# Optimization experiments

Measured on AMD Instinct MI355X. Metric: run time of the kernel, lower is better.

Reference implementation:

```python
import jax, jax.numpy as jnp
import numpy as np

EMBED_DIM = 128
N_HEADS = 8
HEAD_DEPTH = EMBED_DIM // N_HEADS  # 16
CLIP = 10.0
B, N = 256, 1000


def setup_inputs() -> dict:
    key = jax.random.key(0)
    ks = jax.random.split(key, 10)
    D = EMBED_DIM
    return {
        "node_embeddings": jax.random.normal(ks[0], (B, N, D), jnp.float32),
        "graph_embedding": jax.random.normal(ks[1], (B, D), jnp.float32),
        "step_context": jax.random.normal(ks[2], (B, 1, D + 2), jnp.float32),
        "mask": jax.random.randint(ks[3], (B, 1, N), 0, 2).astype(bool),
        "Wk1": jax.random.normal(ks[4], (D, D), jnp.float32) / np.sqrt(D),
        "Wv": jax.random.normal(ks[5], (D, D), jnp.float32) / np.sqrt(D),
        "Wk2": jax.random.normal(ks[6], (D, D), jnp.float32) / np.sqrt(D),
        "Wq_fixed": jax.random.normal(ks[7], (D, D), jnp.float32) / np.sqrt(D),
        "Wout": jax.random.normal(ks[8], (D, D), jnp.float32) / np.sqrt(D),
        "Wq_step": jax.random.normal(ks[9], (D + 2, D), jnp.float32) / np.sqrt(D),
    }


def reference(node_embeddings, graph_embedding, step_context, mask,
              Wk1, Wv, Wk2, Wq_fixed, Wout, Wq_step):
    b, n, D = node_embeddings.shape
    H, dh = N_HEADS, HEAD_DEPTH
    neg_inf = jnp.float32(-1e9)

    # compute_static: precomputed projections of node/graph embeddings
    K1 = node_embeddings @ Wk1                      # [B,N,D]
    V = node_embeddings @ Wv                        # [B,N,D]
    K2 = node_embeddings @ Wk2                      # [B,N,D]
    Q_fixed = graph_embedding[:, None, :] @ Wq_fixed  # [B,1,D]

    # compute_dynamic: single-query masked MHA
    Q_step = step_context @ Wq_step                 # [B,1,D]
    Q1 = Q_fixed + Q_step                           # [B,1,D]
    q = Q1.reshape(b, 1, H, dh)
    k = K1.reshape(b, n, H, dh)
    v = V.reshape(b, n, H, dh)
    score = jnp.einsum('bqhd,bkhd->bhqk', q, k) / jnp.sqrt(jnp.float32(dh))
    score = jnp.where(mask[:, None, :, :], neg_inf, score)  # mask [B,1,N] -> [B,1,1,N]
    attn = jax.nn.softmax(score, axis=-1)           # [B,H,1,N]
    mha = jnp.einsum('bhqk,bkhd->bqhd', attn, v).reshape(b, 1, D)
    Q2 = mha @ Wout                                 # [B,1,D]

    # SHA: clipped single-head logits over all nodes
    logits = CLIP * jnp.tanh(
        jnp.einsum('bqd,bkd->bqk', Q2, K2) / jnp.sqrt(jnp.float32(D)))  # [B,1,N]
    logits = jnp.where(mask, neg_inf, logits)
    return logits[:, 0, :]                          # [B,N]
```

## Files before the change

### kernel.cpp

```cpp
#include <hip/hip_runtime.h>
#include <stdint.h>


#define DD 128
#define NH 8
#define DHD 16
#define NS 8
#define NMAX_PAD 1024
#define TILE 64
#define RP 132

__device__ __forceinline__ bool detect_mask32(const void* maskp) {
    const uint32_t* mw = (const uint32_t*)maskp;
    bool m32 = true;
    #pragma unroll
    for (int i = 0; i < 16; ++i) m32 = m32 && (mw[i] <= 1u);
    return m32;
}

__global__ __launch_bounds__(128)
void k0_prep(const float* __restrict__ graph, const float* __restrict__ ctx,
             const float* __restrict__ Wk1, const float* __restrict__ Wqf,
             const float* __restrict__ Wqs, float* __restrict__ wq_ws)
{
    __shared__ float q1[DD];
    const int b = blockIdx.x, tid = threadIdx.x;
    const float* ge = graph + (size_t)b * DD;
    const float* sc = ctx + (size_t)b * (DD + 2);
    float acc = 0.f;
    for (int k = 0; k < DD; ++k)     acc += ge[k] * Wqf[k * DD + tid];
    for (int k = 0; k < DD + 2; ++k) acc += sc[k] * Wqs[k * DD + tid];
    q1[tid] = acc;
    __syncthreads();
    const float* wrow = Wk1 + (size_t)tid * DD;
    #pragma unroll
    for (int h = 0; h < NH; ++h) {
        float a = 0.f;
        #pragma unroll
        for (int j = 0; j < DHD; ++j) a += wrow[h * DHD + j] * q1[h * DHD + j];
        wq_ws[(size_t)b * NH * DD + h * DD + tid] = 0.25f * a;
    }
}

__global__ __launch_bounds__(512)
void k1_scores(const float* __restrict__ node, const float* __restrict__ wq_ws,
               float* __restrict__ attn_ws, int N)
{
    __shared__ float tile[TILE * RP];
    __shared__ float wq_l[NH * RP];
    const int b = blockIdx.y, tid = threadIdx.x;
    const int base = blockIdx.x * 128;
    const float* nodeB = node + (size_t)b * N * DD;

    for (int i = tid; i < NH * DD; i += 512) {
        const int h = i >> 7, dp = i & 127;
        wq_l[h * RP + dp] = wq_ws[(size_t)b * NH * DD + h * DD + dp];
    }
    __syncthreads();

    const int n_local = tid >> 3, hA = tid & 7;
    for (int t = 0; t < 2; ++t) {
        const int n0 = base + t * TILE;
        #pragma unroll
        for (int c = 0; c < 4; ++c) {
            const int idx = c * (512 * 4) + tid * 4;
            const int row = idx >> 7, col = idx & 127;
            if (n0 + row < N)
                *(float4*)&tile[row * RP + col] =
                    *(const float4*)(nodeB + (size_t)(n0 + row) * DD + col);
        }
        __syncthreads();
        if (n0 + n_local < N) {
            const float4* nr = (const float4*)&tile[n_local * RP];
            const float4* wr = (const float4*)&wq_l[hA * RP];
            float acc = 0.f;
            #pragma unroll
            for (int k = 0; k < 32; ++k) {
                const float4 a = nr[k], w = wr[k];
                acc += a.x * w.x + a.y * w.y + a.z * w.z + a.w * w.w;
            }
            attn_ws[(size_t)b * NH * NMAX_PAD + hA * NMAX_PAD + (n0 + n_local)] = acc;
        }
        __syncthreads();
    }
}

__global__ __launch_bounds__(512)
void k2_softmax(const void* __restrict__ maskp, float* __restrict__ attn_ws, int N)
{
    const int b = blockIdx.x, tid = threadIdx.x, lane = tid & 63, h = tid >> 6;
    const bool m32 = detect_mask32(maskp);
    const int32_t* mi = (const int32_t*)maskp + (size_t)b * N;
    const uint8_t* mb = (const uint8_t*)maskp + (size_t)b * N;
    float* arow = attn_ws + (size_t)b * NH * NMAX_PAD + h * NMAX_PAD;

    float sm[16];
    #pragma unroll
    for (int k = 0; k < 16; ++k) {
        const int n = lane + 64 * k;
        float v = -1e30f;
        if (n < N) {
            const bool m = m32 ? (mi[n] != 0) : (mb[n] != 0);
            v = m ? -1e9f : arow[n];
        }
        sm[k] = v;
    }
    float mx = sm[0];
    #pragma unroll
    for (int k = 1; k < 16; ++k) mx = fmaxf(mx, sm[k]);
    #pragma unroll
    for (int d = 1; d < 64; d <<= 1) mx = fmaxf(mx, __shfl_xor(mx, d));
    float e[16], sum = 0.f;
    #pragma unroll
    for (int k = 0; k < 16; ++k) {
        e[k] = __expf(sm[k] - mx);
        sum += e[k];
    }
    #pragma unroll
    for (int d = 1; d < 64; d <<= 1) sum += __shfl_xor(sum, d);
    const float rinv = 1.f / sum;
    #pragma unroll
    for (int k = 0; k < 16; ++k) {
        const int n = lane + 64 * k;
        if (n < N) arow[n] = e[k] * rinv;
    }
}

__global__ __launch_bounds__(256)
void k3_spart(const float* __restrict__ node, const float* __restrict__ attn_ws,
              float* __restrict__ spart_ws, int N)
{
    __shared__ float at_l[NH * 128];
    __shared__ float red[4 * NH * DD];
    const int b = blockIdx.y, j = blockIdx.x, tid = threadIdx.x;
    const int rows = (N + NS - 1) / NS;
    const int n0 = j * rows;
    const int nrows = min(rows, N - n0);

    for (int h = 0; h < NH; ++h)
        for (int r = tid; r < nrows; r += 256)
            at_l[h * 128 + r] = attn_ws[(size_t)b * NH * NMAX_PAD + h * NMAX_PAD + n0 + r];
    __syncthreads();

    const float* nodeB = node + (size_t)b * N * DD;
    const int c = tid & 63, r0 = tid >> 6;
    float2 acc[NH];
    #pragma unroll
    for (int h = 0; h < NH; ++h) acc[h] = make_float2(0.f, 0.f);
    for (int r = r0; r < nrows; r += 4) {
        const float2 v = *(const float2*)(nodeB + (size_t)(n0 + r) * DD + 2 * c);
        #pragma unroll
        for (int h = 0; h < NH; ++h) {
            const float w = at_l[h * 128 + r];
            acc[h].x += w * v.x;
            acc[h].y += w * v.y;
        }
    }
    #pragma unroll
    for (int h = 0; h < NH; ++h) {
        red[(r0 * NH + h) * DD + 2 * c]     = acc[h].x;
        red[(r0 * NH + h) * DD + 2 * c + 1] = acc[h].y;
    }
    __syncthreads();
    for (int o = tid; o < NH * DD; o += 256) {
        const float s = red[o] + red[NH * DD + o] + red[2 * NH * DD + o] + red[3 * NH * DD + o];
        spart_ws[((size_t)b * NS + j) * NH * DD + o] = s;
    }
}

__global__ __launch_bounds__(128)
void k4_head(const float* __restrict__ spart_ws, const float* __restrict__ Wv,
             const float* __restrict__ Wout, const float* __restrict__ Wk2,
             float* __restrict__ w2_ws)
{
    __shared__ float s_l[NH * DD];
    __shared__ float mha_l[DD];
    __shared__ float q2_l[DD];
    const int b = blockIdx.x, tid = threadIdx.x;
    const float* sp = spart_ws + (size_t)b * NS * NH * DD;
    for (int o = tid; o < NH * DD; o += 128) {
        float s = 0.f;
        #pragma unroll
        for (int j = 0; j < NS; ++j) s += sp[j * NH * DD + o];
        s_l[o] = s;
    }
    __syncthreads();
    {
        const int h = tid >> 4;
        float a = 0.f;
        for (int dp = 0; dp < DD; ++dp) a += s_l[h * DD + dp] * Wv[dp * DD + tid];
        mha_l[tid] = a;
    }
    __syncthreads();
    {
        float a = 0.f;
        for (int e = 0; e < DD; ++e) a += mha_l[e] * Wout[e * DD + tid];
        q2_l[tid] = a;
    }
    __syncthreads();
    {
        const float4* row = (const float4*)(Wk2 + (size_t)tid * DD);
        float a = 0.f;
        #pragma unroll
        for (int k = 0; k < 32; ++k) {
            const float4 w = row[k];
            a += w.x * q2_l[4*k] + w.y * q2_l[4*k+1] + w.z * q2_l[4*k+2] + w.w * q2_l[4*k+3];
        }
        w2_ws[(size_t)b * DD + tid] = a * 0.08838834764831845f;
    }
}

__global__ __launch_bounds__(256)
void k5_logits(const float* __restrict__ node, const float* __restrict__ w2_ws,
               const void* __restrict__ maskp, float* __restrict__ out, int N)
{
    const int b = blockIdx.y, j = blockIdx.x, tid = threadIdx.x;
    const int rows = (N + NS - 1) / NS;
    const int n0 = j * rows;
    const int nend = min(n0 + rows, N);
    const bool m32 = detect_mask32(maskp);
    const int32_t* mi = (const int32_t*)maskp + (size_t)b * N;
    const uint8_t* mb = (const uint8_t*)maskp + (size_t)b * N;
    const int sub = tid & 7, rr = tid >> 3;

    const float4* wv = (const float4*)(w2_ws + (size_t)b * DD + sub * 16);
    const float4 w0 = wv[0], w1 = wv[1], w2v = wv[2], w3 = wv[3];
    const float* nodeB = node + (size_t)b * N * DD;
    float* outB = out + (size_t)b * N;

    for (int n = n0 + rr; n < nend; n += 32) {
        const float4* nr = (const float4*)(nodeB + (size_t)n * DD + sub * 16);
        const float4 a0 = nr[0], a1 = nr[1], a2 = nr[2], a3 = nr[3];
        float p = a0.x*w0.x + a0.y*w0.y + a0.z*w0.z + a0.w*w0.w
                + a1.x*w1.x + a1.y*w1.y + a1.z*w1.z + a1.w*w1.w
                + a2.x*w2v.x + a2.y*w2v.y + a2.z*w2v.z + a2.w*w2v.w
                + a3.x*w3.x + a3.y*w3.y + a3.z*w3.z + a3.w*w3.w;
        p += __shfl_xor(p, 1);
        p += __shfl_xor(p, 2);
        p += __shfl_xor(p, 4);
        if (sub == 0) {
            const bool m = m32 ? (mi[n] != 0) : (mb[n] != 0);
            const float t = 1.f - 2.f / (__expf(2.f * p) + 1.f);
            outB[n] = m ? -1e9f : 10.f * t;
        }
    }
}

#define TPB 512
#define NMAX 1000
#define SPAD 9

__global__ __launch_bounds__(TPB)
void decoder_fallback(const float* __restrict__ node, const float* __restrict__ graph,
                      const float* __restrict__ ctx, const void* __restrict__ maskp,
                      const float* __restrict__ Wk1, const float* __restrict__ Wv,
                      const float* __restrict__ Wk2, const float* __restrict__ Wqf,
                      const float* __restrict__ Wout, const float* __restrict__ Wqs,
                      float* __restrict__ out, int N)
{
    __shared__ float node_tile[TILE * RP];
    __shared__ float scores[NMAX * SPAD];
    __shared__ float wq[NH * RP];
    __shared__ float s_lds[NH * RP];
    __shared__ float q1[DD];
    __shared__ float mha[DD];
    __shared__ float q2[DD];
    __shared__ float w2[DD];

    const int b = blockIdx.x, tid = threadIdx.x, lane = tid & 63, wave = tid >> 6;
    const bool mask32 = detect_mask32(maskp);
    const int32_t* mi = (const int32_t*)maskp + (size_t)b * N;
    const uint8_t* mb = (const uint8_t*)maskp + (size_t)b * N;
    const float* nodeB = node + (size_t)b * N * DD;

    if (tid < DD) {
        const float* ge = graph + (size_t)b * DD;
        const float* sc = ctx + (size_t)b * (DD + 2);
        float acc = 0.f;
        for (int k = 0; k < DD; ++k)     acc += ge[k] * Wqf[k * DD + tid];
        for (int k = 0; k < DD + 2; ++k) acc += sc[k] * Wqs[k * DD + tid];
        q1[tid] = acc;
    }
    __syncthreads();
    for (int idx = tid; idx < NH * DD; idx += TPB) {
        const int h = idx >> 7, dp = idx & (DD - 1);
        const float* wrow = Wk1 + dp * DD + h * DHD;
        float acc = 0.f;
        #pragma unroll
        for (int j = 0; j < DHD; ++j) acc += wrow[j] * q1[h * DHD + j];
        wq[h * RP + dp] = 0.25f * acc;
    }
    __syncthreads();
    const int ntiles = (N + TILE - 1) / TILE;
    const int n_local = tid >> 3, hA = tid & 7;
    for (int t = 0; t < ntiles; ++t) {
        const int n0 = t * TILE;
        #pragma unroll
        for (int c = 0; c < 4; ++c) {
            const int idx = c * (TPB * 4) + tid * 4;
            const int row = idx >> 7, col = idx & (DD - 1);
            if (n0 + row < N)
                *(float4*)&node_tile[row * RP + col] =
                    *(const float4*)(nodeB + (size_t)(n0 + row) * DD + col);
        }
        __syncthreads();
        if (n0 + n_local < N) {
            const float4* nr = (const float4*)&node_tile[n_local * RP];
            const float4* wr = (const float4*)&wq[hA * RP];
            float acc = 0.f;
            #pragma unroll
            for (int k = 0; k < DD / 4; ++k) {
                const float4 a = nr[k], w = wr[k];
                acc += a.x * w.x + a.y * w.y + a.z * w.z + a.w * w.w;
            }
            scores[(n0 + n_local) * SPAD + hA] = acc;
        }
        __syncthreads();
    }
    {
        const int h = wave;
        float sm[16];
        #pragma unroll
        for (int k = 0; k < 16; ++k) {
            const int n = lane + 64 * k;
            float v = -1e9f;
            if (n < N) {
                const bool m = mask32 ? (mi[n] != 0) : (mb[n] != 0);
                v = m ? -1e9f : scores[n * SPAD + h];
            }
            sm[k] = v;
        }
        float mx = sm[0];
        #pragma unroll
        for (int k = 1; k < 16; ++k) mx = fmaxf(mx, sm[k]);
        #pragma unroll
        for (int d = 1; d < 64; d <<= 1) mx = fmaxf(mx, __shfl_xor(mx, d));
        float e[16];
        float sum = 0.f;
        #pragma unroll
        for (int k = 0; k < 16; ++k) {
            const int n = lane + 64 * k;
            e[k] = (n < N) ? __expf(sm[k] - mx) : 0.f;
            sum += e[k];
        }
        #pragma unroll
        for (int d = 1; d < 64; d <<= 1) sum += __shfl_xor(sum, d);
        const float rinv = 1.f / sum;
        #pragma unroll
        for (int k = 0; k < 16; ++k) {
            const int n = lane + 64 * k;
            if (n < N) scores[n * SPAD + h] = e[k] * rinv;
        }
    }
    __syncthreads();
    {
        const int h = wave;
        const float2* n2 = (const float2*)nodeB;
        float a0 = 0.f, a1 = 0.f;
        #pragma unroll 4
        for (int n = 0; n < N; ++n) {
            const float at = scores[n * SPAD + h];
            const float2 v = n2[(size_t)n * 64 + lane];
            a0 += at * v.x;
            a1 += at * v.y;
        }
        s_lds[h * RP + 2 * lane] = a0;
        s_lds[h * RP + 2 * lane + 1] = a1;
    }
    __syncthreads();
    if (tid < DD) {
        const int h = tid >> 4;
        float acc = 0.f;
        for (int dp = 0; dp < DD; ++dp) acc += s_lds[h * RP + dp] * Wv[dp * DD + tid];
        mha[tid] = acc;
    }
    __syncthreads();
    if (tid < DD) {
        float acc = 0.f;
        for (int e = 0; e < DD; ++e) acc += mha[e] * Wout[e * DD + tid];
        q2[tid] = acc;
    }
    __syncthreads();
    if (tid < DD) {
        const float4* row = (const float4*)(Wk2 + tid * DD);
        float acc = 0.f;
        #pragma unroll
        for (int k = 0; k < DD / 4; ++k) {
            const float4 wv = row[k];
            acc += wv.x * q2[4*k] + wv.y * q2[4*k+1] + wv.z * q2[4*k+2] + wv.w * q2[4*k+3];
        }
        w2[tid] = acc * 0.08838834764831845f;
    }
    __syncthreads();
    {
        const float wa = w2[2 * lane], wb = w2[2 * lane + 1];
        const float2* n2 = (const float2*)nodeB;
        float* outB = out + (size_t)b * N;
        for (int n = wave; n < N; n += NH) {
            const float2 v = n2[(size_t)n * 64 + lane];
            float p = v.x * wa + v.y * wb;
            #pragma unroll
            for (int d = 1; d < 64; d <<= 1) p += __shfl_xor(p, d);
            if (lane == 0) {
                const bool m = mask32 ? (mi[n] != 0) : (mb[n] != 0);
                const float t = 1.f - 2.f / (__expf(2.f * p) + 1.f);
                outB[n] = m ? -1e9f : 10.f * t;
            }
        }
    }
}

extern "C" void kernel_launch(void* const* d_in, const int* in_sizes, int n_in,
                              void* d_out, int out_size, void* d_ws, size_t ws_size,
                              hipStream_t stream) {
    (void)n_in; (void)out_size;
    const float* node  = (const float*)d_in[0];
    const float* graph = (const float*)d_in[1];
    const float* ctx   = (const float*)d_in[2];
    const void*  mask  = d_in[3];
    const float* Wk1   = (const float*)d_in[4];
    const float* Wv    = (const float*)d_in[5];
    const float* Wk2   = (const float*)d_in[6];
    const float* Wqf   = (const float*)d_in[7];
    const float* Wout  = (const float*)d_in[8];
    const float* Wqs   = (const float*)d_in[9];

    const int B = in_sizes[1] / DD;
    const int N = in_sizes[0] / (B * DD);

    const size_t off_wq    = 0;
    const size_t off_attn  = off_wq + (size_t)B * NH * DD;
    const size_t off_spart = off_attn + (size_t)B * NH * NMAX_PAD;
    const size_t off_w2    = off_spart + (size_t)B * NS * NH * DD;
    const size_t need_f    = off_w2 + (size_t)B * DD;

    if (N <= NMAX_PAD && ws_size >= need_f * sizeof(float)) {
        float* ws    = (float*)d_ws;
        float* wq_ws    = ws + off_wq;
        float* attn_ws  = ws + off_attn;
        float* spart_ws = ws + off_spart;
        float* w2_ws    = ws + off_w2;

        k0_prep<<<B, 128, 0, stream>>>(graph, ctx, Wk1, Wqf, Wqs, wq_ws);
        k1_scores<<<dim3((N + 127) / 128, B), 512, 0, stream>>>(node, wq_ws, attn_ws, N);
        k2_softmax<<<B, 512, 0, stream>>>(mask, attn_ws, N);
        k3_spart<<<dim3(NS, B), 256, 0, stream>>>(node, attn_ws, spart_ws, N);
        k4_head<<<B, 128, 0, stream>>>(spart_ws, Wv, Wout, Wk2, w2_ws);
        k5_logits<<<dim3(NS, B), 256, 0, stream>>>(node, w2_ws, mask, (float*)d_out, N);
    } else {
        decoder_fallback<<<B, TPB, 0, stream>>>(node, graph, ctx, mask,
                                                Wk1, Wv, Wk2, Wqf, Wout, Wqs,
                                                (float*)d_out, N);
    }
}
```

Before: 112.7 us.

## Fuse score, softmax and value accumulation into a split-N online-softmax kernel

Replaces the separate score, softmax and weighted-sum kernels with one flash-style kernel. Each block handles one eighth of the nodes of a batch and keeps a running max and sum per head, and a small combine kernel merges the partial results using their max/sum statistics. This drops two launches, the attention-score round trip through the workspace, and one of the two reads of node embeddings. In exchange it adds online-rescaling work and a heavier 512-thread block per slice. Loop unroll hints are also added to the prep kernel.

```diff
diff --git a/kernel.cpp b/kernel.cpp
--- a/kernel.cpp
+++ b/kernel.cpp
@@ -6,9 +6,10 @@
 #define NH 8
 #define DHD 16
 #define NS 8
-#define NMAX_PAD 1024
 #define TILE 64
 #define RP 132
+#define SP 9
+#define NMAX_PAD 1024
 
 __device__ __forceinline__ bool detect_mask32(const void* maskp) {
     const uint32_t* mw = (const uint32_t*)maskp;
@@ -28,7 +29,9 @@
     const float* ge = graph + (size_t)b * DD;
     const float* sc = ctx + (size_t)b * (DD + 2);
     float acc = 0.f;
+    #pragma unroll 4
     for (int k = 0; k < DD; ++k)     acc += ge[k] * Wqf[k * DD + tid];
+    #pragma unroll 4
     for (int k = 0; k < DD + 2; ++k) acc += sc[k] * Wqs[k * DD + tid];
     q1[tid] = acc;
     __syncthreads();
@@ -43,145 +46,139 @@
 }
 
 __global__ __launch_bounds__(512)
-void k1_scores(const float* __restrict__ node, const float* __restrict__ wq_ws,
-               float* __restrict__ attn_ws, int N)
+void kA_flash(const float* __restrict__ node, const float* __restrict__ wq_ws,
+              const void* __restrict__ maskp, float* __restrict__ spart_ws,
+              float* __restrict__ mz_ws, int N)
 {
     __shared__ float tile[TILE * RP];
     __shared__ float wq_l[NH * RP];
-    const int b = blockIdx.y, tid = threadIdx.x;
-    const int base = blockIdx.x * 128;
-    const float* nodeB = node + (size_t)b * N * DD;
-
-    for (int i = tid; i < NH * DD; i += 512) {
-        const int h = i >> 7, dp = i & 127;
-        wq_l[h * RP + dp] = wq_ws[(size_t)b * NH * DD + h * DD + dp];
-    }
-    __syncthreads();
-
-    const int n_local = tid >> 3, hA = tid & 7;
-    for (int t = 0; t < 2; ++t) {
-        const int n0 = base + t * TILE;
-        #pragma unroll
-        for (int c = 0; c < 4; ++c) {
-            const int idx = c * (512 * 4) + tid * 4;
-            const int row = idx >> 7, col = idx & 127;
-            if (n0 + row < N)
-                *(float4*)&tile[row * RP + col] =
-                    *(const float4*)(nodeB + (size_t)(n0 + row) * DD + col);
-        }
-        __syncthreads();
-        if (n0 + n_local < N) {
-            const float4* nr = (const float4*)&tile[n_local * RP];
-            const float4* wr = (const float4*)&wq_l[hA * RP];
-            float acc = 0.f;
-            #pragma unroll
-            for (int k = 0; k < 32; ++k) {
-                const float4 a = nr[k], w = wr[k];
-                acc += a.x * w.x + a.y * w.y + a.z * w.z + a.w * w.w;
-            }
-            attn_ws[(size_t)b * NH * NMAX_PAD + hA * NMAX_PAD + (n0 + n_local)] = acc;
-        }
-        __syncthreads();
-    }
-}
-
-__global__ __launch_bounds__(512)
-void k2_softmax(const void* __restrict__ maskp, float* __restrict__ attn_ws, int N)
-{
-    const int b = blockIdx.x, tid = threadIdx.x, lane = tid & 63, h = tid >> 6;
+    __shared__ float s_t[TILE * SP];
+    const int b = blockIdx.y, j = blockIdx.x, tid = threadIdx.x;
+    const int lane = tid & 63, h = tid >> 6;
+    const int rows = (N + NS - 1) / NS;
+    const int n0 = j * rows;
+    const int nend = min(n0 + rows, N);
     const bool m32 = detect_mask32(maskp);
     const int32_t* mi = (const int32_t*)maskp + (size_t)b * N;
     const uint8_t* mb = (const uint8_t*)maskp + (size_t)b * N;
-    float* arow = attn_ws + (size_t)b * NH * NMAX_PAD + h * NMAX_PAD;
-
-    float sm[16];
-    #pragma unroll
-    for (int k = 0; k < 16; ++k) {
-        const int n = lane + 64 * k;
-        float v = -1e30f;
-        if (n < N) {
-            const bool m = m32 ? (mi[n] != 0) : (mb[n] != 0);
-            v = m ? -1e9f : arow[n];
-        }
-        sm[k] = v;
-    }
-    float mx = sm[0];
-    #pragma unroll
-    for (int k = 1; k < 16; ++k) mx = fmaxf(mx, sm[k]);
-    #pragma unroll
-    for (int d = 1; d < 64; d <<= 1) mx = fmaxf(mx, __shfl_xor(mx, d));
-    float e[16], sum = 0.f;
-    #pragma unroll
-    for (int k = 0; k < 16; ++k) {
-        e[k] = __expf(sm[k] - mx);
-        sum += e[k];
-    }
-    #pragma unroll
-    for (int d = 1; d < 64; d <<= 1) sum += __shfl_xor(sum, d);
-    const float rinv = 1.f / sum;
-    #pragma unroll
-    for (int k = 0; k < 16; ++k) {
-        const int n = lane + 64 * k;
-        if (n < N) arow[n] = e[k] * rinv;
-    }
-}
-
-__global__ __launch_bounds__(256)
-void k3_spart(const float* __restrict__ node, const float* __restrict__ attn_ws,
-              float* __restrict__ spart_ws, int N)
+    const float* nodeB = node + (size_t)b * N * DD;
+
+    for (int i = tid; i < NH * DD; i += 512)
+        wq_l[(i >> 7) * RP + (i & 127)] = wq_ws[(size_t)b * NH * DD + i];
+
+    const int r_sc = tid >> 3, h_sc = tid & 7;
+    float m_run = -1e9f, z_run = 0.f;
+    float accx = 0.f, accy = 0.f;
+
+    const int ntiles = (nend - n0 + TILE - 1) / TILE;
+    for (int t = 0; t < ntiles; ++t) {
+        const int nt0 = n0 + t * TILE;
+        #pragma unroll
+        for (int c = 0; c < 4; ++c) {
+            const int idx = c * 2048 + tid * 4;
+            const int row = idx >> 7, col = idx & 127;
+            if (nt0 + row < nend)
+                *(float4*)&tile[row * RP + col] =
+                    *(const float4*)(nodeB + (size_t)(nt0 + row) * DD + col);
+        }
+        __syncthreads();
+        {
+            const int n = nt0 + r_sc;
+            float sc = -1e9f;
+            if (n < nend) {
+                const bool m = m32 ? (mi[n] != 0) : (mb[n] != 0);
+                if (!m) {
+                    const float4* nr = (const float4*)&tile[r_sc * RP];
+                    const float4* wr = (const float4*)&wq_l[h_sc * RP];
+                    float a = 0.f;
+                    #pragma unroll
+                    for (int k = 0; k < 32; ++k) {
+                        const float4 x = nr[k], w = wr[k];
+                        a += x.x * w.x + x.y * w.y + x.z * w.z + x.w * w.w;
+                    }
+                    sc = a;
+                }
+            }
+            s_t[r_sc * SP + h_sc] = sc;
+        }
+        __syncthreads();
+        {
+            float scl = s_t[lane * SP + h];
+            float tmax = scl;
+            #pragma unroll
+            for (int d = 1; d < 64; d <<= 1) tmax = fmaxf(tmax, __shfl_xor(tmax, d));
+            const float m_new = fmaxf(m_run, tmax);
+            const float rescale = __expf(m_run - m_new);
+            const float e = __expf(scl - m_new);
+            s_t[lane * SP + h] = e;
+            float zt = e;
+            #pragma unroll
+            for (int d = 1; d < 64; d <<= 1) zt += __shfl_xor(zt, d);
+            z_run = z_run * rescale + zt;
+            accx *= rescale;
+            accy *= rescale;
+            m_run = m_new;
+        }
+        #pragma unroll 8
+        for (int r = 0; r < TILE; ++r) {
+            const float ef = s_t[r * SP + h];
+            const float2 v = *(const float2*)&tile[r * RP + 2 * lane];
+            accx += ef * v.x;
+            accy += ef * v.y;
+        }
+        __syncthreads();
+    }
+    float* vout = spart_ws + (((size_t)b * NS + j) * NH + h) * DD;
+    vout[2 * lane]     = accx;
+    vout[2 * lane + 1] = accy;
+    if (lane == 0) {
+        float* mzp = mz_ws + (((size_t)b * NS + j) * NH + h) * 2;
+        mzp[0] = m_run;
+        mzp[1] = z_run;
+    }
+}
+
+__global__ __launch_bounds__(128)
+void kB_combine(const float* __restrict__ spart_ws, const float* __restrict__ mz_ws,
+                const float* __restrict__ Wv, const float* __restrict__ Wout,
+                const float* __restrict__ Wk2, float* __restrict__ w2_ws)
 {
-    __shared__ float at_l[NH * 128];
-    __shared__ float red[4 * NH * DD];
-    const int b = blockIdx.y, j = blockIdx.x, tid = threadIdx.x;
-    const int rows = (N + NS - 1) / NS;
-    const int n0 = j * rows;
-    const int nrows = min(rows, N - n0);
-
-    for (int h = 0; h < NH; ++h)
-        for (int r = tid; r < nrows; r += 256)
-            at_l[h * 128 + r] = attn_ws[(size_t)b * NH * NMAX_PAD + h * NMAX_PAD + n0 + r];
-    __syncthreads();
-
-    const float* nodeB = node + (size_t)b * N * DD;
-    const int c = tid & 63, r0 = tid >> 6;
-    float2 acc[NH];
-    #pragma unroll
-    for (int h = 0; h < NH; ++h) acc[h] = make_float2(0.f, 0.f);
-    for (int r = r0; r < nrows; r += 4) {
-        const float2 v = *(const float2*)(nodeB + (size_t)(n0 + r) * DD + 2 * c);
-        #pragma unroll
-        for (int h = 0; h < NH; ++h) {
-            const float w = at_l[h * 128 + r];
-            acc[h].x += w * v.x;
-            acc[h].y += w * v.y;
-        }
-    }
-    #pragma unroll
-    for (int h = 0; h < NH; ++h) {
-        red[(r0 * NH + h) * DD + 2 * c]     = acc[h].x;
-        red[(r0 * NH + h) * DD + 2 * c + 1] = acc[h].y;
-    }
-    __syncthreads();
-    for (int o = tid; o < NH * DD; o += 256) {
-        const float s = red[o] + red[NH * DD + o] + red[2 * NH * DD + o] + red[3 * NH * DD + o];
-        spart_ws[((size_t)b * NS + j) * NH * DD + o] = s;
-    }
-}
-
-__global__ __launch_bounds__(128)
-void k4_head(const float* __restrict__ spart_ws, const float* __restrict__ Wv,
-             const float* __restrict__ Wout, const float* __restrict__ Wk2,
-             float* __restrict__ w2_ws)
-{
+    __shared__ float m_l[NH * NS], z_l[NH * NS], wt[NH * NS];
     __shared__ float s_l[NH * DD];
     __shared__ float mha_l[DD];
     __shared__ float q2_l[DD];
     const int b = blockIdx.x, tid = threadIdx.x;
+
+    if (tid < NH * NS) {
+        const int h = tid >> 3, j = tid & 7;
+        const float* mzp = mz_ws + (((size_t)b * NS + j) * NH + h) * 2;
+        m_l[h * NS + j] = mzp[0];
+        z_l[h * NS + j] = mzp[1];
+    }
+    __syncthreads();
+    if (tid < NH) {
+        const int h = tid;
+        float M = -1e30f;
+        #pragma unroll
+        for (int j = 0; j < NS; ++j) M = fmaxf(M, m_l[h * NS + j]);
+        float w[NS], Z = 0.f;
+        #pragma unroll
+        for (int j = 0; j < NS; ++j) {
+            w[j] = __expf(m_l[h * NS + j] - M);
+            Z += z_l[h * NS + j] * w[j];
+        }
+        const float rz = 1.f / Z;
+        #pragma unroll
+        for (int j = 0; j < NS; ++j) wt[h * NS + j] = w[j] * rz;
+    }
+    __syncthreads();
     const float* sp = spart_ws + (size_t)b * NS * NH * DD;
     for (int o = tid; o < NH * DD; o += 128) {
+        const int h = o >> 7;
         float s = 0.f;
         #pragma unroll
-        for (int j = 0; j < NS; ++j) s += sp[j * NH * DD + o];
+        for (int j = 0; j < NS; ++j)
+            s += sp[(size_t)j * NH * DD + o] * wt[h * NS + j];
         s_l[o] = s;
     }
     __syncthreads();
@@ -429,23 +426,21 @@
     const int N = in_sizes[0] / (B * DD);
 
     const size_t off_wq    = 0;
-    const size_t off_attn  = off_wq + (size_t)B * NH * DD;
-    const size_t off_spart = off_attn + (size_t)B * NH * NMAX_PAD;
-    const size_t off_w2    = off_spart + (size_t)B * NS * NH * DD;
+    const size_t off_spart = off_wq + (size_t)B * NH * DD;
+    const size_t off_mz    = off_spart + (size_t)B * NS * NH * DD;
+    const size_t off_w2    = off_mz + (size_t)B * NS * NH * 2;
     const size_t need_f    = off_w2 + (size_t)B * DD;
 
     if (N <= NMAX_PAD && ws_size >= need_f * sizeof(float)) {
-        float* ws    = (float*)d_ws;
+        float* ws       = (float*)d_ws;
         float* wq_ws    = ws + off_wq;
-        float* attn_ws  = ws + off_attn;
         float* spart_ws = ws + off_spart;
+        float* mz_ws    = ws + off_mz;
         float* w2_ws    = ws + off_w2;
 
         k0_prep<<<B, 128, 0, stream>>>(graph, ctx, Wk1, Wqf, Wqs, wq_ws);
-        k1_scores<<<dim3((N + 127) / 128, B), 512, 0, stream>>>(node, wq_ws, attn_ws, N);
-        k2_softmax<<<B, 512, 0, stream>>>(mask, attn_ws, N);
-        k3_spart<<<dim3(NS, B), 256, 0, stream>>>(node, attn_ws, spart_ws, N);
-        k4_head<<<B, 128, 0, stream>>>(spart_ws, Wv, Wout, Wk2, w2_ws);
+        kA_flash<<<dim3(NS, B), 512, 0, stream>>>(node, wq_ws, mask, spart_ws, mz_ws, N);
+        kB_combine<<<B, 128, 0, stream>>>(spart_ws, mz_ws, Wv, Wout, Wk2, w2_ws);
         k5_logits<<<dim3(NS, B), 256, 0, stream>>>(node, w2_ws, mask, (float*)d_out, N);
     } else {
         decoder_fallback<<<B, TPB, 0, stream>>>(node, graph, ctx, mask,
```

New measurement: 118.6 us. 5.2% more time.
